# Performance work log

Measured on AMD Instinct MI355X. Metric: run time of the kernel, lower is better.

The kernel has to match this reference:

```python
import jax, jax.numpy as jnp
import numpy as np

N_NODES = 80000
N_EDGES = 1280000
D_IN = 64
D_OUT = 64


def setup_inputs() -> dict:
    key = jax.random.key(0)
    k1, k2, k3, k4 = jax.random.split(key, 4)
    x = jax.random.normal(k1, (N_NODES, D_IN), dtype=jnp.float32)
    edge_index = jax.random.randint(k2, (2, N_EDGES), 0, N_NODES, dtype=jnp.int64)
    # GCNConv linear weight (stored as [in, out] for x @ W) and post-aggregation bias
    W = jax.random.normal(k3, (D_IN, D_OUT), dtype=jnp.float32) / jnp.sqrt(jnp.float32(D_IN))
    b = jax.random.normal(k4, (D_OUT,), dtype=jnp.float32) * 0.01
    return {"x": x, "edge_index": edge_index, "W": W, "b": b}


def reference(x, edge_index, W, b):
    # GCNConv (PyG defaults): add self-loops, symmetric normalization,
    # linear transform, scatter-add aggregation, bias; then ReLU.
    N = x.shape[0]
    loops = jnp.arange(N, dtype=edge_index.dtype)
    src = jnp.concatenate([edge_index[0], loops])  # [E+N]
    dst = jnp.concatenate([edge_index[1], loops])  # [E+N]

    # degree over destination nodes (self-loops included -> deg >= 1)
    deg = jax.ops.segment_sum(jnp.ones_like(src, dtype=x.dtype), dst, num_segments=N)
    dinv = jax.lax.rsqrt(jnp.where(deg > 0, deg, jnp.ones_like(deg)))
    norm = dinv[src] * dinv[dst]  # [E+N]

    h = x @ W  # [N, D_OUT]
    msg = h[src] * norm[:, None]  # gather + scale, [E+N, D_OUT]
    agg = jax.ops.segment_sum(msg, dst, num_segments=N)  # scatter-add, [N, D_OUT]
    return jax.nn.relu(agg + b)
```

## Files before the change

kernel.cpp:

```cpp
#include <hip/hip_runtime.h>
#include <hip/hip_bf16.h>

#define D 64
#define NODES_PER_BIN 256
#define BIN_SHIFT 8
#define CAP 5120
#define TILE 4096
#define EPT 16
#define WSTR 72

typedef short bf16x8 __attribute__((ext_vector_type(8)));
typedef float f32x4 __attribute__((ext_vector_type(4)));

__device__ __forceinline__ float bf2f(unsigned short u) {
    union { unsigned int i; float f; } c; c.i = (unsigned int)u << 16; return c.f;
}
__device__ __forceinline__ unsigned short f2bf(float f) {
    union { float f; unsigned int i; } c; c.f = f;
    unsigned int x = c.i;
    return (unsigned short)((x + 0x7fffu + ((x >> 16) & 1u)) >> 16);
}


__global__ __launch_bounds__(256) void k_hist(const int* __restrict__ dst, int* __restrict__ binCount,
                                              int E, int NBINS) {
    __shared__ int h[512];
    int tid = threadIdx.x;
    for (int i = tid; i < 512; i += 256) h[i] = 0;
    __syncthreads();
    for (long long i = (long long)blockIdx.x * 256 + tid; i < E; i += (long long)gridDim.x * 256)
        atomicAdd(&h[dst[(int)i] >> BIN_SHIFT], 1);
    __syncthreads();
    for (int i = tid; i < NBINS; i += 256) if (h[i]) atomicAdd(&binCount[i], h[i]);
}

__global__ __launch_bounds__(256) void k_binscan(const int* __restrict__ binCount,
                                                 int* __restrict__ bin_base,
                                                 int* __restrict__ bin_cursor, int NBINS) {
    __shared__ int sA[512], sB[512];
    int tid = threadIdx.x;
    for (int i = tid; i < 512; i += 256) sA[i] = (i < NBINS) ? binCount[i] : 0;
    __syncthreads();
    int *a = sA, *bb = sB;
    for (int dd = 1; dd < 512; dd <<= 1) {
        for (int i = tid; i < 512; i += 256) bb[i] = a[i] + (i >= dd ? a[i - dd] : 0);
        __syncthreads();
        int* t = a; a = bb; bb = t;
    }
    for (int i = tid; i < NBINS; i += 256) {
        int v = (i > 0) ? a[i - 1] : 0;
        bin_base[i] = v;
        bin_cursor[i] = v;
    }
}

__global__ __launch_bounds__(256) void k_passA(const int* __restrict__ src,
                                               const int* __restrict__ dst,
                                               int* __restrict__ bin_cursor,
                                               int* __restrict__ binned,
                                               int E, int NBINS) {
    __shared__ int hist[512];
    __shared__ int localBase[512];
    __shared__ int reservedBase[512];
    __shared__ int sA[512], sB[512];
    __shared__ int stagVal[TILE];
    __shared__ int stagDst[TILE];
    int tid = threadIdx.x;
    long long t0 = (long long)blockIdx.x * TILE;
    int cnt_tile = (int)((E - t0 < TILE) ? (E - t0) : TILE);

    for (int i = tid; i < 512; i += 256) hist[i] = 0;
    __syncthreads();

    int val[EPT]; int bn[EPT];
#pragma unroll
    for (int k = 0; k < EPT; ++k) {
        int i = k * 256 + tid;
        if (i < cnt_tile) {
            int e = (int)t0 + i;
            int s = src[e], d = dst[e];
            bn[k] = d >> BIN_SHIFT;
            val[k] = s | ((d & (NODES_PER_BIN - 1)) << 17);
            atomicAdd(&hist[bn[k]], 1);
        } else { bn[k] = -1; val[k] = 0; }
    }
    __syncthreads();

    for (int i = tid; i < 512; i += 256) sA[i] = hist[i];
    __syncthreads();
    int *a = sA, *bb = sB;
    for (int dd = 1; dd < 512; dd <<= 1) {
        for (int i = tid; i < 512; i += 256) bb[i] = a[i] + (i >= dd ? a[i - dd] : 0);
        __syncthreads();
        int* t = a; a = bb; bb = t;
    }
    for (int i = tid; i < 512; i += 256) localBase[i] = (i > 0 ? a[i - 1] : 0);
    for (int i = tid; i < NBINS; i += 256) reservedBase[i] = atomicAdd(&bin_cursor[i], hist[i]);
    __syncthreads();
    for (int i = tid; i < 512; i += 256) hist[i] = 0;
    __syncthreads();
#pragma unroll
    for (int k = 0; k < EPT; ++k) {
        if (bn[k] >= 0) {
            int r = atomicAdd(&hist[bn[k]], 1);
            int slot = localBase[bn[k]] + r;
            stagVal[slot] = val[k];
            stagDst[slot] = reservedBase[bn[k]] + r;
        }
    }
    __syncthreads();
    for (int i = tid; i < cnt_tile; i += 256) binned[stagDst[i]] = stagVal[i];
}

__global__ __launch_bounds__(256) void k_passB(const int* __restrict__ binned,
                                               const int* __restrict__ bin_base,
                                               const int* __restrict__ binCount,
                                               int* __restrict__ sorted_src,
                                               int* __restrict__ row_ptr,
                                               int* __restrict__ counts,
                                               float* __restrict__ dinv, int N) {
    __shared__ int eLDS[CAP];
    __shared__ int srt[CAP];
    __shared__ int cnt[NODES_PER_BIN];
    __shared__ int nodeOff[NODES_PER_BIN];
    __shared__ int sA[NODES_PER_BIN], sB[NODES_PER_BIN];
    int tid = threadIdx.x;
    int b = blockIdx.x;
    int lo = b << BIN_SHIFT;
    int nNodes = N - lo; if (nNodes > NODES_PER_BIN) nNodes = NODES_PER_BIN;
    int base = bin_base[b];
    int size = binCount[b]; if (size > CAP) size = CAP;

    for (int i = tid; i < size; i += 256) eLDS[i] = binned[base + i];
    cnt[tid] = 0;
    __syncthreads();
    for (int i = tid; i < size; i += 256) atomicAdd(&cnt[eLDS[i] >> 17], 1);
    __syncthreads();
    sA[tid] = cnt[tid];
    __syncthreads();
    int *a = sA, *bb = sB;
    for (int dd = 1; dd < 256; dd <<= 1) {
        bb[tid] = a[tid] + (tid >= dd ? a[tid - dd] : 0);
        __syncthreads();
        int* t = a; a = bb; bb = t;
    }
    nodeOff[tid] = (tid > 0) ? a[tid - 1] : 0;
    __syncthreads();
    if (tid < nNodes) {
        int c = cnt[tid];
        row_ptr[lo + tid] = base + nodeOff[tid];
        counts[lo + tid] = c;
        dinv[lo + tid] = rsqrtf(1.0f + (float)c);
    }
    __syncthreads();
    cnt[tid] = 0;
    __syncthreads();
    for (int i = tid; i < size; i += 256) {
        int v = eLDS[i];
        int dl = v >> 17;
        int r = atomicAdd(&cnt[dl], 1);
        srt[nodeOff[dl] + r] = v & 0x1FFFF;
    }
    __syncthreads();
    for (int i = tid; i < size; i += 256) sorted_src[base + i] = srt[i];
}

__global__ __launch_bounds__(256) void k_gemm_v3(const float* __restrict__ x,
                                                 const float* __restrict__ W,
                                                 const float* __restrict__ dinv,
                                                 unsigned short* __restrict__ g, int N) {
    __shared__ unsigned short WtHi[D * WSTR];
    __shared__ unsigned short WtLo[D * WSTR];
    int tid = threadIdx.x;
    for (int idx = tid; idx < D * D; idx += 256) {
        int k = idx >> 6, j = idx & 63;
        float w = W[idx];
        unsigned short hi = f2bf(w);
        WtHi[j * WSTR + k] = hi;
        WtLo[j * WSTR + k] = f2bf(w - bf2f(hi));
    }
    __syncthreads();

    int lane = tid & 63;
    int wid  = tid >> 6;
    int r0 = (blockIdx.x * 4 + wid) * 16;
    if (r0 >= N) return;

    int lcol = lane & 15;
    int lkg  = lane >> 4;

    bf16x8 Bhi[2][4], Blo[2][4];
#pragma unroll
    for (int s = 0; s < 2; ++s)
#pragma unroll
        for (int n = 0; n < 4; ++n) {
            int j = n * 16 + lcol;
            int k = s * 32 + lkg * 8;
            Bhi[s][n] = *(const bf16x8*)&WtHi[j * WSTR + k];
            Blo[s][n] = *(const bf16x8*)&WtLo[j * WSTR + k];
        }

    int arow = r0 + lcol;
    bool rok = (arow < N);
    bf16x8 Ahi[2], Alo[2];
#pragma unroll
    for (int s = 0; s < 2; ++s) {
        float4 v0{0.f,0.f,0.f,0.f}, v1{0.f,0.f,0.f,0.f};
        if (rok) {
            const float4* p = (const float4*)&x[(size_t)arow * D + s * 32 + lkg * 8];
            v0 = p[0]; v1 = p[1];
        }
        float xv[8] = {v0.x, v0.y, v0.z, v0.w, v1.x, v1.y, v1.z, v1.w};
#pragma unroll
        for (int e = 0; e < 8; ++e) {
            unsigned short hi = f2bf(xv[e]);
            Ahi[s][e] = (short)hi;
            Alo[s][e] = (short)f2bf(xv[e] - bf2f(hi));
        }
    }

    f32x4 acc[4];
#pragma unroll
    for (int n = 0; n < 4; ++n) {
        f32x4 c = {0.f, 0.f, 0.f, 0.f};
        c = __builtin_amdgcn_mfma_f32_16x16x32_bf16(Ahi[0], Bhi[0][n], c, 0, 0, 0);
        c = __builtin_amdgcn_mfma_f32_16x16x32_bf16(Ahi[1], Bhi[1][n], c, 0, 0, 0);
        c = __builtin_amdgcn_mfma_f32_16x16x32_bf16(Alo[0], Bhi[0][n], c, 0, 0, 0);
        c = __builtin_amdgcn_mfma_f32_16x16x32_bf16(Alo[1], Bhi[1][n], c, 0, 0, 0);
        c = __builtin_amdgcn_mfma_f32_16x16x32_bf16(Ahi[0], Blo[0][n], c, 0, 0, 0);
        c = __builtin_amdgcn_mfma_f32_16x16x32_bf16(Ahi[1], Blo[1][n], c, 0, 0, 0);
        acc[n] = c;
    }

#pragma unroll
    for (int i = 0; i < 4; ++i) {
        int orow = r0 + lkg * 4 + i;
        if (orow < N) {
            float dv = dinv[orow];
#pragma unroll
            for (int n = 0; n < 4; ++n)
                g[(size_t)orow * D + n * 16 + lcol] = f2bf(acc[n][i] * dv);
        }
    }
}

__global__ __launch_bounds__(256) void k_aggregate6(const int* __restrict__ row_ptr,
                                                    const int* __restrict__ counts,
                                                    const int* __restrict__ sorted_src,
                                                    const ushort4* __restrict__ g4,
                                                    const float* __restrict__ dinv,
                                                    const float* __restrict__ b,
                                                    float* __restrict__ out, int N) {
    int n = (blockIdx.x * 256 + threadIdx.x) >> 6;
    int lane = threadIdx.x & 63;
    if (n >= N) return;
    int q = lane >> 4;
    int p = lane & 15;
    int start = row_ptr[n];
    int cnt = counts[n];
    const int* sp = sorted_src + start;

    float a0 = 0.f, a1 = 0.f, a2 = 0.f, a3 = 0.f;
    if (q == 0) {
        ushort4 v = g4[(size_t)n * 16 + p];
        a0 = bf2f(v.x); a1 = bf2f(v.y); a2 = bf2f(v.z); a3 = bf2f(v.w);
    }

#define LIDX(jg, I, M)                                         \
    {                                                          \
        int e_ = (jg) * 4 + q;                                 \
        bool ok_ = (e_ < cnt);                                 \
        I = ok_ ? sp[e_] : n;                                  \
        M = ok_ ? 1.f : 0.f;                                   \
    }
#define CONS(V, M)                                             \
    {                                                          \
        a0 = fmaf(M, bf2f(V.x), a0);                           \
        a1 = fmaf(M, bf2f(V.y), a1);                           \
        a2 = fmaf(M, bf2f(V.z), a2);                           \
        a3 = fmaf(M, bf2f(V.w), a3);                           \
    }

    int i0, i1, i2, i3, i4, i5, i6, i7;
    float m0, m1, m2, m3, m4, m5, m6, m7;
    LIDX(0, i0, m0); LIDX(1, i1, m1); LIDX(2, i2, m2); LIDX(3, i3, m3);
    LIDX(4, i4, m4); LIDX(5, i5, m5); LIDX(6, i6, m6); LIDX(7, i7, m7);
    ushort4 u0 = g4[(size_t)i0 * 16 + p];
    ushort4 u1 = g4[(size_t)i1 * 16 + p];
    ushort4 u2 = g4[(size_t)i2 * 16 + p];
    ushort4 u3 = g4[(size_t)i3 * 16 + p];
    ushort4 u4 = g4[(size_t)i4 * 16 + p];
    ushort4 u5 = g4[(size_t)i5 * 16 + p];
    ushort4 u6 = g4[(size_t)i6 * 16 + p];
    ushort4 u7 = g4[(size_t)i7 * 16 + p];
    CONS(u0, m0); CONS(u1, m1); CONS(u2, m2); CONS(u3, m3);
    CONS(u4, m4); CONS(u5, m5); CONS(u6, m6); CONS(u7, m7);

    int ng = (cnt + 3) >> 2;
    for (int jg = 8; jg < ng; ++jg) {
        int I; float M;
        LIDX(jg, I, M);
        ushort4 U = g4[(size_t)I * 16 + p];
        CONS(U, M);
    }
#undef LIDX
#undef CONS

    a0 += __shfl_xor(a0, 16, 64); a0 += __shfl_xor(a0, 32, 64);
    a1 += __shfl_xor(a1, 16, 64); a1 += __shfl_xor(a1, 32, 64);
    a2 += __shfl_xor(a2, 16, 64); a2 += __shfl_xor(a2, 32, 64);
    a3 += __shfl_xor(a3, 16, 64); a3 += __shfl_xor(a3, 32, 64);

    if (q == 0) {
        float dv = dinv[n];
        float4 bias = ((const float4*)b)[p];
        float4 r;
        r.x = fmaxf(fmaf(a0, dv, bias.x), 0.f);
        r.y = fmaxf(fmaf(a1, dv, bias.y), 0.f);
        r.z = fmaxf(fmaf(a2, dv, bias.z), 0.f);
        r.w = fmaxf(fmaf(a3, dv, bias.w), 0.f);
        ((float4*)out)[(size_t)n * 16 + p] = r;
    }
}


__global__ void k_deg_init(float* __restrict__ deg, int N) {
    int i = blockIdx.x * blockDim.x + threadIdx.x;
    if (i < N) deg[i] = 1.0f;
}
__global__ void k_deg_count(const int* __restrict__ dst, float* __restrict__ deg, int E) {
    int i = blockIdx.x * blockDim.x + threadIdx.x;
    if (i < E) atomicAdd(&deg[dst[i]], 1.0f);
}
__global__ void k_dinv_f(float* __restrict__ deg, int N) {
    int i = blockIdx.x * blockDim.x + threadIdx.x;
    if (i < N) deg[i] = rsqrtf(deg[i]);
}
__global__ __launch_bounds__(256) void k_gemm_fb(const float* __restrict__ x, const float* __restrict__ W,
                                                 const float* __restrict__ dinv, float* __restrict__ g,
                                                 float* __restrict__ acc, int N) {
    __shared__ float Ws[D * D];
    __shared__ float xs[4][D];
    int tid = threadIdx.x;
    for (int t = tid; t < D * D; t += 256) Ws[t] = W[t];
    int rg = tid >> 6, j = tid & 63;
    int r = blockIdx.x * 4 + rg;
    if (r < N) xs[rg][j] = x[r * D + j];
    __syncthreads();
    if (r < N) {
        float s = 0.f;
#pragma unroll
        for (int k = 0; k < D; ++k) s = fmaf(xs[rg][k], Ws[k * D + j], s);
        s *= dinv[r];
        g[r * D + j] = s;
        acc[r * D + j] = s;
    }
}
__global__ __launch_bounds__(256) void k_scatter_fb(const int* __restrict__ src, const int* __restrict__ dst,
                                                    const float* __restrict__ g, float* __restrict__ acc, int E) {
    long long idx = (long long)blockIdx.x * blockDim.x + threadIdx.x;
    int e = (int)(idx >> 6), j = (int)(idx & 63);
    if (e < E) atomicAdd(&acc[dst[e] * D + j], g[src[e] * D + j]);
}
__global__ void k_final_fb(float* __restrict__ out, const float* __restrict__ dinv,
                           const float* __restrict__ b, int N) {
    int idx = blockIdx.x * blockDim.x + threadIdx.x;
    if (idx < N * D) {
        int r = idx >> 6, j = idx & 63;
        float v = out[idx] * dinv[r] + b[j];
        out[idx] = v > 0.f ? v : 0.f;
    }
}


extern "C" void kernel_launch(void* const* d_in, const int* in_sizes, int n_in,
                              void* d_out, int out_size, void* d_ws, size_t ws_size,
                              hipStream_t stream) {
    const float* x  = (const float*)d_in[0];
    const int*   ei = (const int*)d_in[1];
    const float* W  = (const float*)d_in[2];
    const float* b  = (const float*)d_in[3];
    float* out = (float*)d_out;

    const int N = in_sizes[0] / D;
    const int E = in_sizes[1] / 2;
    const int* src = ei;
    const int* dst = ei + E;
    const int NBINS = (N + NODES_PER_BIN - 1) >> BIN_SHIFT;

    size_t off = 0;
    auto take = [&](size_t bytes) { size_t p = off; off = (off + bytes + 255) & ~(size_t)255; return p; };
    char* base = (char*)d_ws;
    size_t o_counts  = take((size_t)N * 4);
    size_t o_dinv    = take((size_t)N * 4);
    size_t o_rowptr  = take((size_t)N * 4);
    size_t o_binc    = take(512 * 4);
    size_t o_binb    = take(512 * 4);
    size_t o_bincur  = take(512 * 4);
    size_t o_sorted  = take((size_t)E * 4);
    size_t o_binned  = take((size_t)E * 4);
    size_t o_g       = take((size_t)N * D * 2);
    size_t req1 = off;

    bool tier1_ok = (ws_size >= req1) && (N <= (1 << 17)) && (NBINS <= 512);

    if (tier1_ok) {
        int* counts     = (int*)(base + o_counts);
        float* dinv     = (float*)(base + o_dinv);
        int* row_ptr    = (int*)(base + o_rowptr);
        int* binCount   = (int*)(base + o_binc);
        int* bin_base   = (int*)(base + o_binb);
        int* bin_cursor = (int*)(base + o_bincur);
        int* sorted_src = (int*)(base + o_sorted);
        int* binned     = (int*)(base + o_binned);
        unsigned short* g = (unsigned short*)(base + o_g);

        hipMemsetAsync(binCount, 0, (size_t)NBINS * 4, stream);
        k_hist<<<512, 256, 0, stream>>>(dst, binCount, E, NBINS);
        k_binscan<<<1, 256, 0, stream>>>(binCount, bin_base, bin_cursor, NBINS);
        k_passA<<<(E + TILE - 1) / TILE, 256, 0, stream>>>(src, dst, bin_cursor, binned, E, NBINS);
        k_passB<<<NBINS, 256, 0, stream>>>(binned, bin_base, binCount, sorted_src, row_ptr, counts, dinv, N);
        {
            int nTiles = (N + 15) / 16;
            int gemmBlocks = (nTiles + 3) / 4;
            k_gemm_v3<<<gemmBlocks, 256, 0, stream>>>(x, W, dinv, g, N);
        }
        long long thr = (long long)N * 64;
        k_aggregate6<<<(int)((thr + 255) / 256), 256, 0, stream>>>(row_ptr, counts, sorted_src,
                                                                   (const ushort4*)g, dinv, b, out, N);
        return;
    }

    {
        float* deg = (float*)d_ws;
        float* g   = (float*)((char*)d_ws + (size_t)N * sizeof(float));
        k_deg_init<<<(N + 255) / 256, 256, 0, stream>>>(deg, N);
        k_deg_count<<<(E + 255) / 256, 256, 0, stream>>>(dst, deg, E);
        k_dinv_f<<<(N + 255) / 256, 256, 0, stream>>>(deg, N);
        k_gemm_fb<<<(N + 3) / 4, 256, 0, stream>>>(x, W, deg, g, out, N);
        long long total = (long long)E * D;
        k_scatter_fb<<<(int)((total + 255) / 256), 256, 0, stream>>>(src, dst, g, out, E);
        k_final_fb<<<(N * D + 255) / 256, 256, 0, stream>>>(out, deg, b, N);
    }
}
```

Before: 102.2 us.

## Replace prefix-scanned bin offsets with fixed-capacity bins, dropping histogram and scan kernels

Each destination bin now gets a fixed slot range of CAP entries, so pass A can reserve space with per-bin atomic cursors starting at zero. This removes the separate histogram kernel, the single-block bin scan kernel and their extra read of the dst array. Pass B reads its bin at b*CAP and uses the cursor as the bin count. The staging tile is also halved to 2048 edges with 8 edges per thread, giving more, smaller blocks. The cost is workspace sized NBINS*CAP instead of E. A bin holding more than CAP edges would now write into the next bin's slots instead of only being truncated.

```diff
diff --git a/kernel.cpp b/kernel.cpp
--- a/kernel.cpp
+++ b/kernel.cpp
@@ -5,8 +5,8 @@
 #define NODES_PER_BIN 256
 #define BIN_SHIFT 8
 #define CAP 5120
-#define TILE 4096
-#define EPT 16
+#define TILE 2048
+#define EPT 8
 #define WSTR 72
 
 typedef short bf16x8 __attribute__((ext_vector_type(8)));
@@ -21,42 +21,9 @@
     return (unsigned short)((x + 0x7fffu + ((x >> 16) & 1u)) >> 16);
 }
 
-
-__global__ __launch_bounds__(256) void k_hist(const int* __restrict__ dst, int* __restrict__ binCount,
-                                              int E, int NBINS) {
-    __shared__ int h[512];
-    int tid = threadIdx.x;
-    for (int i = tid; i < 512; i += 256) h[i] = 0;
-    __syncthreads();
-    for (long long i = (long long)blockIdx.x * 256 + tid; i < E; i += (long long)gridDim.x * 256)
-        atomicAdd(&h[dst[(int)i] >> BIN_SHIFT], 1);
-    __syncthreads();
-    for (int i = tid; i < NBINS; i += 256) if (h[i]) atomicAdd(&binCount[i], h[i]);
-}
-
-__global__ __launch_bounds__(256) void k_binscan(const int* __restrict__ binCount,
-                                                 int* __restrict__ bin_base,
-                                                 int* __restrict__ bin_cursor, int NBINS) {
-    __shared__ int sA[512], sB[512];
-    int tid = threadIdx.x;
-    for (int i = tid; i < 512; i += 256) sA[i] = (i < NBINS) ? binCount[i] : 0;
-    __syncthreads();
-    int *a = sA, *bb = sB;
-    for (int dd = 1; dd < 512; dd <<= 1) {
-        for (int i = tid; i < 512; i += 256) bb[i] = a[i] + (i >= dd ? a[i - dd] : 0);
-        __syncthreads();
-        int* t = a; a = bb; bb = t;
-    }
-    for (int i = tid; i < NBINS; i += 256) {
-        int v = (i > 0) ? a[i - 1] : 0;
-        bin_base[i] = v;
-        bin_cursor[i] = v;
-    }
-}
-
 __global__ __launch_bounds__(256) void k_passA(const int* __restrict__ src,
                                                const int* __restrict__ dst,
-                                               int* __restrict__ bin_cursor,
+                                               int* __restrict__ cursor,
                                                int* __restrict__ binned,
                                                int E, int NBINS) {
     __shared__ int hist[512];
@@ -95,7 +62,8 @@
         int* t = a; a = bb; bb = t;
     }
     for (int i = tid; i < 512; i += 256) localBase[i] = (i > 0 ? a[i - 1] : 0);
-    for (int i = tid; i < NBINS; i += 256) reservedBase[i] = atomicAdd(&bin_cursor[i], hist[i]);
+    for (int i = tid; i < NBINS; i += 256)
+        reservedBase[i] = (hist[i] > 0) ? atomicAdd(&cursor[i], hist[i]) : 0;
     __syncthreads();
     for (int i = tid; i < 512; i += 256) hist[i] = 0;
     __syncthreads();
@@ -105,7 +73,7 @@
             int r = atomicAdd(&hist[bn[k]], 1);
             int slot = localBase[bn[k]] + r;
             stagVal[slot] = val[k];
-            stagDst[slot] = reservedBase[bn[k]] + r;
+            stagDst[slot] = bn[k] * CAP + reservedBase[bn[k]] + r;
         }
     }
     __syncthreads();
@@ -113,7 +81,6 @@
 }
 
 __global__ __launch_bounds__(256) void k_passB(const int* __restrict__ binned,
-                                               const int* __restrict__ bin_base,
                                                const int* __restrict__ binCount,
                                                int* __restrict__ sorted_src,
                                                int* __restrict__ row_ptr,
@@ -128,7 +95,7 @@
     int b = blockIdx.x;
     int lo = b << BIN_SHIFT;
     int nNodes = N - lo; if (nNodes > NODES_PER_BIN) nNodes = NODES_PER_BIN;
-    int base = bin_base[b];
+    int base = b * CAP;
     int size = binCount[b]; if (size > CAP) size = CAP;
 
     for (int i = tid; i < size; i += 256) eLDS[i] = binned[base + i];
@@ -394,11 +361,9 @@
     size_t o_counts  = take((size_t)N * 4);
     size_t o_dinv    = take((size_t)N * 4);
     size_t o_rowptr  = take((size_t)N * 4);
-    size_t o_binc    = take(512 * 4);
-    size_t o_binb    = take(512 * 4);
-    size_t o_bincur  = take(512 * 4);
-    size_t o_sorted  = take((size_t)E * 4);
-    size_t o_binned  = take((size_t)E * 4);
+    size_t o_cursor  = take(512 * 4);
+    size_t o_sorted  = take((size_t)NBINS * CAP * 4);
+    size_t o_binned  = take((size_t)NBINS * CAP * 4);
     size_t o_g       = take((size_t)N * D * 2);
     size_t req1 = off;
 
@@ -408,18 +373,14 @@
         int* counts     = (int*)(base + o_counts);
         float* dinv     = (float*)(base + o_dinv);
         int* row_ptr    = (int*)(base + o_rowptr);
-        int* binCount   = (int*)(base + o_binc);
-        int* bin_base   = (int*)(base + o_binb);
-        int* bin_cursor = (int*)(base + o_bincur);
+        int* cursor     = (int*)(base + o_cursor);
         int* sorted_src = (int*)(base + o_sorted);
         int* binned     = (int*)(base + o_binned);
         unsigned short* g = (unsigned short*)(base + o_g);
 
-        hipMemsetAsync(binCount, 0, (size_t)NBINS * 4, stream);
-        k_hist<<<512, 256, 0, stream>>>(dst, binCount, E, NBINS);
-        k_binscan<<<1, 256, 0, stream>>>(binCount, bin_base, bin_cursor, NBINS);
-        k_passA<<<(E + TILE - 1) / TILE, 256, 0, stream>>>(src, dst, bin_cursor, binned, E, NBINS);
-        k_passB<<<NBINS, 256, 0, stream>>>(binned, bin_base, binCount, sorted_src, row_ptr, counts, dinv, N);
+        hipMemsetAsync(cursor, 0, (size_t)NBINS * 4, stream);
+        k_passA<<<(E + TILE - 1) / TILE, 256, 0, stream>>>(src, dst, cursor, binned, E, NBINS);
+        k_passB<<<NBINS, 256, 0, stream>>>(binned, cursor, sorted_src, row_ptr, counts, dinv, N);
         {
             int nTiles = (N + 15) / 16;
             int gemmBlocks = (nTiles + 3) / 4;
```

Result: faster. 90.36 us (-11.6%).
